# Optimization experiments

Measured on AMD Instinct MI355X. Metric: run time of the kernel, lower is better.

Reference implementation:

```python
import jax, jax.numpy as jnp
import numpy as np

B, D, H, A, T = 2048, 512, 512, 18, 16
W_SCALE = 1e-3


def setup_inputs() -> dict:
    key = jax.random.key(0)
    ks = jax.random.split(key, 7)
    xs = jax.random.normal(ks[0], (B, D), dtype=jnp.float32)
    task_id = jax.random.randint(ks[1], (B,), 0, T)
    action = jax.random.randint(ks[2], (B,), 0, A)
    W1 = jax.random.normal(ks[3], (T, D, H), dtype=jnp.float32) * W_SCALE
    b1 = jnp.zeros((T, H), dtype=jnp.float32)
    W2 = jax.random.normal(ks[4], (T, H, A), dtype=jnp.float32) * W_SCALE
    b2 = jnp.zeros((T, A), dtype=jnp.float32)
    return {"xs": xs, "W1": W1, "b1": b1, "W2": W2, "b2": b2,
            "task_id": task_id, "action": action}


def reference(xs, W1, b1, W2, b2, task_id, action):
    # MultiLinear fc1: gather per-sample weight by task_id, batched matmul
    h = jnp.einsum('bd,bdh->bh', xs, W1[task_id]) + b1[task_id]   # [B, H]
    h = jax.nn.relu(h)
    # MultiLinear fc2 -> logits
    logits = jnp.einsum('bh,bha->ba', h, W2[task_id]) + b2[task_id]  # [B, A]
    # Categorical log_prob / entropy
    logp = jax.nn.log_softmax(logits, axis=-1)                       # [B, A]
    log_pi_a = jnp.take_along_axis(logp, action[:, None], axis=-1)   # [B, 1]
    ent = -jnp.sum(jnp.exp(logp) * logp, axis=-1, keepdims=True)     # [B, 1]
    return action, log_pi_a, ent
```

## Files before the change

kernel.cpp:

```cpp
#include <hip/hip_runtime.h>
#include <math.h>

#define B_ 2048
#define D_ 512
#define H_ 512
#define A_ 18
#define T_ 16
#define MTF 16
#define MAXTILESF 144
#define NSLOT 24

typedef __attribute__((ext_vector_type(8))) short short8;
typedef __attribute__((ext_vector_type(4))) float f32x4;

#define W2T_OFF  (3 << 20)
#define W1T_OFF  (4 << 20)
#define WS_NEED  (12 << 20)

__device__ __forceinline__ unsigned short f2bf(float f) {
    union { float f; unsigned int u; } v; v.f = f;
    unsigned int u = v.u;
    return (unsigned short)((u + 0x7fffu + ((u >> 16) & 1u)) >> 16);
}

__global__ __launch_bounds__(256) void nk_prep(const float* __restrict__ W1,
                                               const float* __restrict__ W2,
                                               const int* __restrict__ task_id,
                                               unsigned short* __restrict__ w1t,
                                               unsigned short* __restrict__ w2t,
                                               int* __restrict__ wsi) {
    int bid = blockIdx.x;
    int tid = threadIdx.x;
    if (bid < 1024) {
        __shared__ float tile[64][65];
        int hx = bid & 7, dy = (bid >> 3) & 7, t = bid >> 6;
        int cx = tid & 63, ry = tid >> 6;
        const float* src = W1 + ((size_t)t * D_ + dy * 64) * H_ + hx * 64;
#pragma unroll
        for (int i = 0; i < 16; ++i) {
            int row = i * 4 + ry;
            tile[row][cx] = src[(size_t)row * H_ + cx];
        }
        __syncthreads();
        unsigned short* dst = w1t + ((size_t)t * H_ + hx * 64) * D_ + dy * 64;
        int c4 = tid & 15, hr0 = tid >> 4;
#pragma unroll
        for (int i = 0; i < 4; ++i) {
            int hr = hr0 + i * 16;
            unsigned short uu[4] = { f2bf(tile[c4 * 4 + 0][hr]), f2bf(tile[c4 * 4 + 1][hr]),
                                     f2bf(tile[c4 * 4 + 2][hr]), f2bf(tile[c4 * 4 + 3][hr]) };
            *(uint2*)(dst + (size_t)hr * D_ + c4 * 4) = *(const uint2*)uu;
        }
    } else if (bid < 1040) {
        int t = bid - 1024;
        const float* src = W2 + (size_t)t * H_ * A_;
        unsigned short* dst = w2t + (size_t)t * 32 * H_;
#pragma unroll
        for (int i = 0; i < 2; ++i) {
            int h = tid * 2 + i;
            float v[A_];
#pragma unroll
            for (int a = 0; a < A_; ++a) v[a] = src[(size_t)h * A_ + a];
#pragma unroll
            for (int a = 0; a < A_; ++a) dst[(size_t)a * H_ + h] = f2bf(v[a]);
#pragma unroll
            for (int a = A_; a < 32; ++a) dst[(size_t)a * H_ + h] = 0;
        }
    } else {
        __shared__ int cnt[T_], cur[T_], soff[T_];
        if (tid < T_) { cnt[tid] = 0; cur[tid] = 0; }
        __syncthreads();
        for (int b = tid; b < B_; b += 256) atomicAdd(&cnt[task_id[b]], 1);
        __syncthreads();
        if (tid == 0) {
            int off = 0;
            for (int t = 0; t < T_; ++t) {
                soff[t] = off; wsi[17 + t] = off;
                off += cnt[t];
            }
            wsi[17 + T_] = off;
        }
        __syncthreads();
        for (int b = tid; b < B_; b += 256) {
            int t = task_id[b];
            int pos = atomicAdd(&cur[t], 1);
            wsi[256 + soff[t] + pos] = b;
        }
    }
}

__global__ __launch_bounds__(512) void nk_fused(
        const float* __restrict__ xs,
        const unsigned short* __restrict__ w1t,
        const unsigned short* __restrict__ w2t,
        const float* __restrict__ b1, const float* __restrict__ b2,
        const int* __restrict__ action, float* __restrict__ out,
        const int* __restrict__ wsi) {
    __shared__ unsigned short x_lds[16][520];
    __shared__ unsigned short h_lds[16][520];
    __shared__ float lg_lds[16][34];
    __shared__ int sidx[16];

    int c = blockIdx.x;
    int tid = threadIdx.x, lane = tid & 63, w = tid >> 6;
    int r15 = lane & 15, kg = lane >> 4;

    int o0 = wsi[17 + c],     n0 = wsi[18 + c] - o0;
    int o1 = wsi[17 + c + 8], n1 = wsi[18 + c + 8] - o1;
    int nt0 = (n0 + 15) >> 4, nt1 = (n1 + 15) >> 4;
    int ntot = nt0 + nt1;

    for (int u = blockIdx.y; u < ntot; u += NSLOT) {
        int t, kt, off0, rT;
        if (u < nt0) { t = c; kt = u; off0 = o0; rT = n0; }
        else { t = c + 8; kt = u - nt0; off0 = o1; rT = n1; }
        int rowbase = off0 + kt * 16;
        int rows = rT - kt * 16; if (rows > 16) rows = 16;

        if (tid < 16) sidx[tid] = wsi[256 + rowbase + (tid < rows ? tid : rows - 1)];
        __syncthreads();

        {
            int row = tid >> 5, col = (tid & 31) * 16;
            const float* src = xs + (size_t)sidx[row] * D_ + col;
            float4 v0 = *(const float4*)(src);
            float4 v1 = *(const float4*)(src + 4);
            float4 v2 = *(const float4*)(src + 8);
            float4 v3 = *(const float4*)(src + 12);
            unsigned short uu[16] = {
                f2bf(v0.x), f2bf(v0.y), f2bf(v0.z), f2bf(v0.w),
                f2bf(v1.x), f2bf(v1.y), f2bf(v1.z), f2bf(v1.w),
                f2bf(v2.x), f2bf(v2.y), f2bf(v2.z), f2bf(v2.w),
                f2bf(v3.x), f2bf(v3.y), f2bf(v3.z), f2bf(v3.w) };
            *(uint4*)&x_lds[row][col]     = *(const uint4*)&uu[0];
            *(uint4*)&x_lds[row][col + 8] = *(const uint4*)&uu[8];
        }
        __syncthreads();

        const unsigned short* bbase = w1t + (size_t)t * H_ * D_ + kg * 8;
        const unsigned short* bp0 = bbase + (size_t)(w * 64 + r15) * D_;
        const unsigned short* bp1 = bp0 + (size_t)16 * D_;
        const unsigned short* bp2 = bp0 + (size_t)32 * D_;
        const unsigned short* bp3 = bp0 + (size_t)48 * D_;

        f32x4 acc0 = {0.f,0.f,0.f,0.f}, acc1 = {0.f,0.f,0.f,0.f};
        f32x4 acc2 = {0.f,0.f,0.f,0.f}, acc3 = {0.f,0.f,0.f,0.f};
#pragma unroll
        for (int ks = 0; ks < 16; ++ks) {
            short8 af = *(const short8*)&x_lds[r15][ks * 32 + kg * 8];
            short8 b0 = *(const short8*)(bp0 + ks * 32);
            short8 b1f = *(const short8*)(bp1 + ks * 32);
            short8 b2f = *(const short8*)(bp2 + ks * 32);
            short8 b3f = *(const short8*)(bp3 + ks * 32);
            acc0 = __builtin_amdgcn_mfma_f32_16x16x32_bf16(af, b0, acc0, 0, 0, 0);
            acc1 = __builtin_amdgcn_mfma_f32_16x16x32_bf16(af, b1f, acc1, 0, 0, 0);
            acc2 = __builtin_amdgcn_mfma_f32_16x16x32_bf16(af, b2f, acc2, 0, 0, 0);
            acc3 = __builtin_amdgcn_mfma_f32_16x16x32_bf16(af, b3f, acc3, 0, 0, 0);
        }

        int colb = w * 64 + r15;
        float bv0 = b1[t * H_ + colb];
        float bv1 = b1[t * H_ + colb + 16];
        float bv2 = b1[t * H_ + colb + 32];
        float bv3 = b1[t * H_ + colb + 48];
#pragma unroll
        for (int j = 0; j < 4; ++j) {
            int row = kg * 4 + j;
            float v;
            v = acc0[j] + bv0; h_lds[row][colb]      = f2bf(v > 0.f ? v : 0.f);
            v = acc1[j] + bv1; h_lds[row][colb + 16] = f2bf(v > 0.f ? v : 0.f);
            v = acc2[j] + bv2; h_lds[row][colb + 32] = f2bf(v > 0.f ? v : 0.f);
            v = acc3[j] + bv3; h_lds[row][colb + 48] = f2bf(v > 0.f ? v : 0.f);
        }
        __syncthreads();

        if (w < 2) {
            const unsigned short* wa = w2t + (size_t)t * 32 * H_
                                       + (size_t)(w * 16 + r15) * H_ + kg * 8;
            f32x4 c0 = {0.f,0.f,0.f,0.f};
#pragma unroll
            for (int ks = 0; ks < 16; ++ks) {
                short8 hf = *(const short8*)&h_lds[r15][ks * 32 + kg * 8];
                short8 w0 = *(const short8*)(wa + ks * 32);
                c0 = __builtin_amdgcn_mfma_f32_16x16x32_bf16(hf, w0, c0, 0, 0, 0);
            }
            int a = w * 16 + r15;
            float bb = (a < A_) ? b2[t * A_ + a] : 0.f;
#pragma unroll
            for (int j = 0; j < 4; ++j) {
                lg_lds[kg * 4 + j][a] = c0[j] + bb;
            }
        }
        __syncthreads();

        if (tid < rows) {
            int b = sidx[tid];
            float logits[A_];
            float m = -1e30f;
#pragma unroll
            for (int a = 0; a < A_; ++a) {
                logits[a] = lg_lds[tid][a];
                m = fmaxf(m, logits[a]);
            }
            float S = 0.f, sle = 0.f;
#pragma unroll
            for (int a = 0; a < A_; ++a) {
                float e = expf(logits[a] - m);
                S += e;
                sle += logits[a] * e;
            }
            float logZ = m + logf(S);
            int as = action[b];
            out[b] = (float)as;
            out[B_ + b] = logits[as] - logZ;
            out[2 * B_ + b] = logZ - sle / S;
        }
        __syncthreads();
    }
}


__global__ void nk_init(int* wsi) { int i = threadIdx.x; if (i < 50) wsi[i] = 0; }

__global__ void nk_count(const int* task_id, int* wsi) {
    int b = blockIdx.x * blockDim.x + threadIdx.x;
    if (b < B_) atomicAdd(&wsi[1 + task_id[b]], 1);
}

__global__ void nk_plan(int* wsi) {
    int off = 0, tot = 0;
    for (int t = 0; t < T_; ++t) {
        wsi[17 + t] = off;
        int cnt = wsi[1 + t];
        int nt = (cnt + MTF - 1) / MTF;
        for (int k = 0; k < nt; ++k) wsi[50 + tot++] = (t << 16) | k;
        off += cnt;
    }
    wsi[17 + T_] = off;
    wsi[0] = tot;
}

__global__ void nk_scatter(const int* task_id, int* wsi) {
    int b = blockIdx.x * blockDim.x + threadIdx.x;
    if (b < B_) {
        int t = task_id[b];
        int pos = atomicAdd(&wsi[34 + t], 1);
        wsi[256 + wsi[17 + t] + pos] = b;
    }
}

__global__ __launch_bounds__(512) void nk_main(
        const float* __restrict__ xs, const float* __restrict__ W1,
        const float* __restrict__ b1, const float* __restrict__ W2,
        const float* __restrict__ b2, const int* __restrict__ task_id,
        const int* __restrict__ action, float* __restrict__ out,
        const int* __restrict__ wsi) {
    __shared__ float tile[MTF][D_];
    __shared__ int sidx[MTF];
    int bid = blockIdx.x;
    if (bid >= wsi[0]) return;
    int code = wsi[50 + bid];
    int t = code >> 16, kt = code & 0xffff;
    int off0 = wsi[17 + t], off1 = wsi[17 + t + 1];
    int base = off0 + kt * MTF;
    int rows = off1 - base; if (rows > MTF) rows = MTF;
    int tid = threadIdx.x;
    if (tid < MTF) sidx[tid] = (tid < rows) ? wsi[256 + base + tid] : -1;
    __syncthreads();
    for (int i = 0; i < MTF; ++i) {
        int b = sidx[i];
        tile[i][tid] = (b >= 0) ? xs[(size_t)b * D_ + tid] : 0.f;
    }
    __syncthreads();
    const float* w1p = W1 + (size_t)t * D_ * H_ + tid;
    float acc[MTF];
#pragma unroll
    for (int i = 0; i < MTF; ++i) acc[i] = 0.f;
    for (int d = 0; d < D_; d += 4) {
        float w0 = w1p[(size_t)(d + 0) * H_];
        float w1v = w1p[(size_t)(d + 1) * H_];
        float w2v = w1p[(size_t)(d + 2) * H_];
        float w3v = w1p[(size_t)(d + 3) * H_];
#pragma unroll
        for (int i = 0; i < MTF; ++i) {
            float4 x = *(const float4*)&tile[i][d];
            float a0 = fmaf(x.x, w0, acc[i]);
            a0 = fmaf(x.y, w1v, a0);
            a0 = fmaf(x.z, w2v, a0);
            acc[i] = fmaf(x.w, w3v, a0);
        }
    }
    __syncthreads();
    float b1v = b1[t * H_ + tid];
#pragma unroll
    for (int i = 0; i < MTF; ++i) {
        float h = acc[i] + b1v;
        tile[i][tid] = h > 0.f ? h : 0.f;
    }
    __syncthreads();
    int g = tid >> 5, l = tid & 31;
    float lg[A_];
#pragma unroll
    for (int a = 0; a < A_; ++a) lg[a] = 0.f;
    const float* w2base = W2 + (size_t)t * H_ * A_;
    for (int hh = l; hh < H_; hh += 32) {
        float hv = tile[g][hh];
        const float* wrow = w2base + (size_t)hh * A_;
#pragma unroll
        for (int a = 0; a < A_; ++a) lg[a] = fmaf(hv, wrow[a], lg[a]);
    }
#pragma unroll
    for (int a = 0; a < A_; ++a) {
        lg[a] += __shfl_down(lg[a], 16, 32);
        lg[a] += __shfl_down(lg[a], 8, 32);
        lg[a] += __shfl_down(lg[a], 4, 32);
        lg[a] += __shfl_down(lg[a], 2, 32);
        lg[a] += __shfl_down(lg[a], 1, 32);
    }
    if (l == 0 && g < rows) {
        int b = sidx[g];
        float logits[A_];
        float m = -1e30f;
#pragma unroll
        for (int a = 0; a < A_; ++a) {
            logits[a] = lg[a] + b2[t * A_ + a];
            m = fmaxf(m, logits[a]);
        }
        float S = 0.f, sle = 0.f;
#pragma unroll
        for (int a = 0; a < A_; ++a) {
            float e = expf(logits[a] - m);
            S += e;
            sle += logits[a] * e;
        }
        float logZ = m + logf(S);
        int as = action[b];
        out[b] = (float)as;
        out[B_ + b] = logits[as] - logZ;
        out[2 * B_ + b] = logZ - sle / S;
    }
}

extern "C" void kernel_launch(void* const* d_in, const int* in_sizes, int n_in,
                              void* d_out, int out_size, void* d_ws, size_t ws_size,
                              hipStream_t stream) {
    const float* xs = (const float*)d_in[0];
    const float* W1 = (const float*)d_in[1];
    const float* b1 = (const float*)d_in[2];
    const float* W2 = (const float*)d_in[3];
    const float* b2 = (const float*)d_in[4];
    const int* task_id = (const int*)d_in[5];
    const int* action = (const int*)d_in[6];
    float* out = (float*)d_out;

    if (ws_size >= WS_NEED) {
        unsigned char* wsb = (unsigned char*)d_ws;
        int* wsi = (int*)d_ws;
        unsigned short* w2t = (unsigned short*)(wsb + W2T_OFF);
        unsigned short* w1t = (unsigned short*)(wsb + W1T_OFF);

        nk_prep<<<1041, 256, 0, stream>>>(W1, W2, task_id, w1t, w2t, wsi);
        nk_fused<<<dim3(8, NSLOT), 512, 0, stream>>>(xs, w1t, w2t, b1, b2,
                                                     action, out, wsi);
    } else {
        int* wsi = (int*)d_ws;
        nk_init<<<1, 64, 0, stream>>>(wsi);
        nk_count<<<(B_ + 255) / 256, 256, 0, stream>>>(task_id, wsi);
        nk_plan<<<1, 1, 0, stream>>>(wsi);
        nk_scatter<<<(B_ + 255) / 256, 256, 0, stream>>>(task_id, wsi);
        nk_main<<<MAXTILESF, 512, 0, stream>>>(xs, W1, b1, W2, b2, task_id, action, out, wsi);
    }
}
```

Measured before the change: 31.40 us.

## Split hidden dim across blocks with partial fc2 sums and separate softmax kernel

The fused per-16-row kernel is replaced by a GEMM kernel in which each block owns one task and a 32-column slice of the hidden dimension. It loops over that task's rows in 64-row tiles and writes partial fc2 logits to a workspace buffer. A new final kernel sums the 16 partials per row, adds b2, and computes log-softmax, log-prob and entropy. Each W1 slice is now loaded once per block instead of once per 16-row tile. The cost is an extra kernel launch, a partial-sum buffer round-trip through global memory, redundant conversion of x in every block, and a larger workspace requirement.

```diff
diff --git a/kernel.cpp b/kernel.cpp
--- a/kernel.cpp
+++ b/kernel.cpp
@@ -8,14 +8,14 @@
 #define T_ 16
 #define MTF 16
 #define MAXTILESF 144
-#define NSLOT 24
 
 typedef __attribute__((ext_vector_type(8))) short short8;
 typedef __attribute__((ext_vector_type(4))) float f32x4;
 
-#define W2T_OFF  (3 << 20)
-#define W1T_OFF  (4 << 20)
-#define WS_NEED  (12 << 20)
+#define PART_OFF 16384
+#define W2T_OFF  (5 << 20)
+#define W1T_OFF  (6 << 20)
+#define WS_NEED  (14 << 20)
 
 __device__ __forceinline__ unsigned short f2bf(float f) {
     union { float f; unsigned int u; } v; v.f = f;
@@ -89,134 +89,146 @@
     }
 }
 
-__global__ __launch_bounds__(512) void nk_fused(
+__global__ __launch_bounds__(256, 2) void nk_gemm(
         const float* __restrict__ xs,
         const unsigned short* __restrict__ w1t,
         const unsigned short* __restrict__ w2t,
-        const float* __restrict__ b1, const float* __restrict__ b2,
-        const int* __restrict__ action, float* __restrict__ out,
+        const float* __restrict__ b1,
+        float* __restrict__ part,
         const int* __restrict__ wsi) {
-    __shared__ unsigned short x_lds[16][520];
-    __shared__ unsigned short h_lds[16][520];
-    __shared__ float lg_lds[16][34];
-    __shared__ int sidx[16];
+    __shared__ unsigned short x_lds[64][520];
+    __shared__ unsigned short h_lds[64][36];
+    __shared__ int sidx[64];
 
     int c = blockIdx.x;
+    int slot = blockIdx.y;
+    int t = c + (slot >> 4) * 8;
+    int cq = slot & 15;
+    int c0 = cq * 32;
+
+    int o = wsi[17 + t];
+    int n = wsi[18 + t] - o;
+
     int tid = threadIdx.x, lane = tid & 63, w = tid >> 6;
     int r15 = lane & 15, kg = lane >> 4;
 
-    int o0 = wsi[17 + c],     n0 = wsi[18 + c] - o0;
-    int o1 = wsi[17 + c + 8], n1 = wsi[18 + c + 8] - o1;
-    int nt0 = (n0 + 15) >> 4, nt1 = (n1 + 15) >> 4;
-    int ntot = nt0 + nt1;
-
-    for (int u = blockIdx.y; u < ntot; u += NSLOT) {
-        int t, kt, off0, rT;
-        if (u < nt0) { t = c; kt = u; off0 = o0; rT = n0; }
-        else { t = c + 8; kt = u - nt0; off0 = o1; rT = n1; }
-        int rowbase = off0 + kt * 16;
-        int rows = rT - kt * 16; if (rows > 16) rows = 16;
-
-        if (tid < 16) sidx[tid] = wsi[256 + rowbase + (tid < rows ? tid : rows - 1)];
+    const unsigned short* bp0 = w1t + (size_t)t * H_ * D_ + (size_t)(c0 + r15) * D_ + kg * 8;
+    const unsigned short* bp1 = bp0 + (size_t)16 * D_;
+    const unsigned short* wa0 = w2t + (size_t)t * 32 * H_ + (size_t)r15 * H_ + c0 + kg * 8;
+    const unsigned short* wa1 = wa0 + (size_t)16 * H_;
+    float bv0 = b1[t * H_ + c0 + r15];
+    float bv1 = b1[t * H_ + c0 + 16 + r15];
+
+    for (int mb = 0; mb * 64 < n; ++mb) {
+        int rowbase = o + mb * 64;
+        int rows = n - mb * 64; if (rows > 64) rows = 64;
+
+        if (tid < 64) sidx[tid] = wsi[256 + rowbase + (tid < rows ? tid : rows - 1)];
         __syncthreads();
 
         {
-            int row = tid >> 5, col = (tid & 31) * 16;
-            const float* src = xs + (size_t)sidx[row] * D_ + col;
-            float4 v0 = *(const float4*)(src);
-            float4 v1 = *(const float4*)(src + 4);
-            float4 v2 = *(const float4*)(src + 8);
-            float4 v3 = *(const float4*)(src + 12);
-            unsigned short uu[16] = {
-                f2bf(v0.x), f2bf(v0.y), f2bf(v0.z), f2bf(v0.w),
-                f2bf(v1.x), f2bf(v1.y), f2bf(v1.z), f2bf(v1.w),
-                f2bf(v2.x), f2bf(v2.y), f2bf(v2.z), f2bf(v2.w),
-                f2bf(v3.x), f2bf(v3.y), f2bf(v3.z), f2bf(v3.w) };
-            *(uint4*)&x_lds[row][col]     = *(const uint4*)&uu[0];
-            *(uint4*)&x_lds[row][col + 8] = *(const uint4*)&uu[8];
-        }
-        __syncthreads();
-
-        const unsigned short* bbase = w1t + (size_t)t * H_ * D_ + kg * 8;
-        const unsigned short* bp0 = bbase + (size_t)(w * 64 + r15) * D_;
-        const unsigned short* bp1 = bp0 + (size_t)16 * D_;
-        const unsigned short* bp2 = bp0 + (size_t)32 * D_;
-        const unsigned short* bp3 = bp0 + (size_t)48 * D_;
+            int row = tid >> 2, cb = (tid & 3) * 128;
+            const float* src = xs + (size_t)sidx[row] * D_ + cb;
+#pragma unroll
+            for (int j = 0; j < 8; ++j) {
+                float4 v0 = *(const float4*)(src + j * 16);
+                float4 v1 = *(const float4*)(src + j * 16 + 4);
+                float4 v2 = *(const float4*)(src + j * 16 + 8);
+                float4 v3 = *(const float4*)(src + j * 16 + 12);
+                unsigned short uu[16] = {
+                    f2bf(v0.x), f2bf(v0.y), f2bf(v0.z), f2bf(v0.w),
+                    f2bf(v1.x), f2bf(v1.y), f2bf(v1.z), f2bf(v1.w),
+                    f2bf(v2.x), f2bf(v2.y), f2bf(v2.z), f2bf(v2.w),
+                    f2bf(v3.x), f2bf(v3.y), f2bf(v3.z), f2bf(v3.w) };
+                *(uint4*)&x_lds[row][cb + j * 16]     = *(const uint4*)&uu[0];
+                *(uint4*)&x_lds[row][cb + j * 16 + 8] = *(const uint4*)&uu[8];
+            }
+        }
+        __syncthreads();
 
         f32x4 acc0 = {0.f,0.f,0.f,0.f}, acc1 = {0.f,0.f,0.f,0.f};
-        f32x4 acc2 = {0.f,0.f,0.f,0.f}, acc3 = {0.f,0.f,0.f,0.f};
 #pragma unroll
         for (int ks = 0; ks < 16; ++ks) {
-            short8 af = *(const short8*)&x_lds[r15][ks * 32 + kg * 8];
+            short8 af = *(const short8*)&x_lds[w * 16 + r15][ks * 32 + kg * 8];
             short8 b0 = *(const short8*)(bp0 + ks * 32);
             short8 b1f = *(const short8*)(bp1 + ks * 32);
-            short8 b2f = *(const short8*)(bp2 + ks * 32);
-            short8 b3f = *(const short8*)(bp3 + ks * 32);
             acc0 = __builtin_amdgcn_mfma_f32_16x16x32_bf16(af, b0, acc0, 0, 0, 0);
             acc1 = __builtin_amdgcn_mfma_f32_16x16x32_bf16(af, b1f, acc1, 0, 0, 0);
-            acc2 = __builtin_amdgcn_mfma_f32_16x16x32_bf16(af, b2f, acc2, 0, 0, 0);
-            acc3 = __builtin_amdgcn_mfma_f32_16x16x32_bf16(af, b3f, acc3, 0, 0, 0);
-        }
-
-        int colb = w * 64 + r15;
-        float bv0 = b1[t * H_ + colb];
-        float bv1 = b1[t * H_ + colb + 16];
-        float bv2 = b1[t * H_ + colb + 32];
-        float bv3 = b1[t * H_ + colb + 48];
+        }
+
 #pragma unroll
         for (int j = 0; j < 4; ++j) {
-            int row = kg * 4 + j;
+            int row = w * 16 + kg * 4 + j;
             float v;
-            v = acc0[j] + bv0; h_lds[row][colb]      = f2bf(v > 0.f ? v : 0.f);
-            v = acc1[j] + bv1; h_lds[row][colb + 16] = f2bf(v > 0.f ? v : 0.f);
-            v = acc2[j] + bv2; h_lds[row][colb + 32] = f2bf(v > 0.f ? v : 0.f);
-            v = acc3[j] + bv3; h_lds[row][colb + 48] = f2bf(v > 0.f ? v : 0.f);
-        }
-        __syncthreads();
-
-        if (w < 2) {
-            const unsigned short* wa = w2t + (size_t)t * 32 * H_
-                                       + (size_t)(w * 16 + r15) * H_ + kg * 8;
-            f32x4 c0 = {0.f,0.f,0.f,0.f};
-#pragma unroll
-            for (int ks = 0; ks < 16; ++ks) {
-                short8 hf = *(const short8*)&h_lds[r15][ks * 32 + kg * 8];
-                short8 w0 = *(const short8*)(wa + ks * 32);
-                c0 = __builtin_amdgcn_mfma_f32_16x16x32_bf16(hf, w0, c0, 0, 0, 0);
+            v = acc0[j] + bv0; h_lds[row][r15]      = f2bf(v > 0.f ? v : 0.f);
+            v = acc1[j] + bv1; h_lds[row][16 + r15] = f2bf(v > 0.f ? v : 0.f);
+        }
+        __syncthreads();
+
+        {
+            short8 hf = *(const short8*)&h_lds[w * 16 + r15][kg * 8];
+            short8 w2f0 = *(const short8*)wa0;
+            short8 w2f1 = *(const short8*)wa1;
+            f32x4 p0 = {0.f,0.f,0.f,0.f}, p1 = {0.f,0.f,0.f,0.f};
+            p0 = __builtin_amdgcn_mfma_f32_16x16x32_bf16(hf, w2f0, p0, 0, 0, 0);
+            p1 = __builtin_amdgcn_mfma_f32_16x16x32_bf16(hf, w2f1, p1, 0, 0, 0);
+#pragma unroll
+            for (int j = 0; j < 4; ++j) {
+                int lrow = w * 16 + kg * 4 + j;
+                if (lrow < rows) {
+                    float* pp = part + ((size_t)(rowbase + lrow) * 16 + cq) * 32;
+                    pp[r15] = p0[j];
+                    pp[16 + r15] = p1[j];
+                }
             }
-            int a = w * 16 + r15;
-            float bb = (a < A_) ? b2[t * A_ + a] : 0.f;
-#pragma unroll
-            for (int j = 0; j < 4; ++j) {
-                lg_lds[kg * 4 + j][a] = c0[j] + bb;
-            }
-        }
-        __syncthreads();
-
-        if (tid < rows) {
-            int b = sidx[tid];
-            float logits[A_];
-            float m = -1e30f;
-#pragma unroll
-            for (int a = 0; a < A_; ++a) {
-                logits[a] = lg_lds[tid][a];
-                m = fmaxf(m, logits[a]);
-            }
-            float S = 0.f, sle = 0.f;
-#pragma unroll
-            for (int a = 0; a < A_; ++a) {
-                float e = expf(logits[a] - m);
-                S += e;
-                sle += logits[a] * e;
-            }
-            float logZ = m + logf(S);
-            int as = action[b];
-            out[b] = (float)as;
-            out[B_ + b] = logits[as] - logZ;
-            out[2 * B_ + b] = logZ - sle / S;
-        }
-        __syncthreads();
-    }
+        }
+        __syncthreads();
+    }
+}
+
+__global__ __launch_bounds__(256) void nk_final(const float* __restrict__ part,
+                                                const float* __restrict__ b2,
+                                                const int* __restrict__ action,
+                                                float* __restrict__ out,
+                                                const int* __restrict__ wsi) {
+    int r = blockIdx.x * 256 + threadIdx.x;
+    if (r >= B_) return;
+    int t = 0;
+#pragma unroll
+    for (int i = 1; i < T_; ++i) t += (r >= wsi[17 + i]) ? 1 : 0;
+    int b = wsi[256 + r];
+
+    float logits[A_];
+#pragma unroll
+    for (int a = 0; a < A_; ++a) logits[a] = b2[t * A_ + a];
+    const float* pr = part + (size_t)r * 16 * 32;
+#pragma unroll
+    for (int cq = 0; cq < 16; ++cq) {
+        const float* pc = pr + cq * 32;
+#pragma unroll
+        for (int a4 = 0; a4 < 5; ++a4) {
+            float4 v = *(const float4*)(pc + a4 * 4);
+            if (a4 * 4 + 0 < A_) logits[a4 * 4 + 0] += v.x;
+            if (a4 * 4 + 1 < A_) logits[a4 * 4 + 1] += v.y;
+            if (a4 * 4 + 2 < A_) logits[a4 * 4 + 2] += v.z;
+            if (a4 * 4 + 3 < A_) logits[a4 * 4 + 3] += v.w;
+        }
+    }
+    float m = -1e30f;
+#pragma unroll
+    for (int a = 0; a < A_; ++a) m = fmaxf(m, logits[a]);
+    float S = 0.f, sle = 0.f;
+#pragma unroll
+    for (int a = 0; a < A_; ++a) {
+        float e = expf(logits[a] - m);
+        S += e;
+        sle += logits[a] * e;
+    }
+    float logZ = m + logf(S);
+    int as = action[b];
+    out[b] = (float)as;
+    out[B_ + b] = logits[as] - logZ;
+    out[2 * B_ + b] = logZ - sle / S;
 }
 
 
@@ -356,12 +368,13 @@
     if (ws_size >= WS_NEED) {
         unsigned char* wsb = (unsigned char*)d_ws;
         int* wsi = (int*)d_ws;
+        float* part = (float*)(wsb + PART_OFF);
         unsigned short* w2t = (unsigned short*)(wsb + W2T_OFF);
         unsigned short* w1t = (unsigned short*)(wsb + W1T_OFF);
 
         nk_prep<<<1041, 256, 0, stream>>>(W1, W2, task_id, w1t, w2t, wsi);
-        nk_fused<<<dim3(8, NSLOT), 512, 0, stream>>>(xs, w1t, w2t, b1, b2,
-                                                     action, out, wsi);
+        nk_gemm<<<dim3(8, 32), 256, 0, stream>>>(xs, w1t, w2t, b1, part, wsi);
+        nk_final<<<(B_ + 255) / 256, 256, 0, stream>>>(part, b2, action, out, wsi);
     } else {
         int* wsi = (int*)d_ws;
         nk_init<<<1, 64, 0, stream>>>(wsi);
```

After: 48.84 us. 1.56x slower.

## Prefetch fc1 MFMA operands and split fc2 K-dimension across four waves

Applied to the files above, without the earlier changes.

The fc1 MFMA loop now software-pipelines its operand loads, fetching the next k-step's x fragment and W1 fragments before issuing the current MFMAs, so global-load latency can hide behind matrix work. The fc2 logits stage moves from two waves each covering the full K=512 to four waves that each handle a quarter of K for both 16-column output tiles. Partial sums go to a per-wave LDS buffer and are reduced, with the bias added, in the softmax thread. This trades more LDS traffic, higher register pressure from the prefetch buffers, and a serial 4-way reduction for a shorter fc2 critical path.

```diff
diff --git a/kernel.cpp b/kernel.cpp
--- a/kernel.cpp
+++ b/kernel.cpp
@@ -98,7 +98,7 @@
         const int* __restrict__ wsi) {
     __shared__ unsigned short x_lds[16][520];
     __shared__ unsigned short h_lds[16][520];
-    __shared__ float lg_lds[16][34];
+    __shared__ float lg_lds[4][16][36];
     __shared__ int sidx[16];
 
     int c = blockIdx.x;
@@ -145,17 +145,29 @@
 
         f32x4 acc0 = {0.f,0.f,0.f,0.f}, acc1 = {0.f,0.f,0.f,0.f};
         f32x4 acc2 = {0.f,0.f,0.f,0.f}, acc3 = {0.f,0.f,0.f,0.f};
+
+        short8 a_cur = *(const short8*)&x_lds[r15][kg * 8];
+        short8 b0c = *(const short8*)(bp0);
+        short8 b1c = *(const short8*)(bp1);
+        short8 b2c = *(const short8*)(bp2);
+        short8 b3c = *(const short8*)(bp3);
 #pragma unroll
         for (int ks = 0; ks < 16; ++ks) {
-            short8 af = *(const short8*)&x_lds[r15][ks * 32 + kg * 8];
-            short8 b0 = *(const short8*)(bp0 + ks * 32);
-            short8 b1f = *(const short8*)(bp1 + ks * 32);
-            short8 b2f = *(const short8*)(bp2 + ks * 32);
-            short8 b3f = *(const short8*)(bp3 + ks * 32);
-            acc0 = __builtin_amdgcn_mfma_f32_16x16x32_bf16(af, b0, acc0, 0, 0, 0);
-            acc1 = __builtin_amdgcn_mfma_f32_16x16x32_bf16(af, b1f, acc1, 0, 0, 0);
-            acc2 = __builtin_amdgcn_mfma_f32_16x16x32_bf16(af, b2f, acc2, 0, 0, 0);
-            acc3 = __builtin_amdgcn_mfma_f32_16x16x32_bf16(af, b3f, acc3, 0, 0, 0);
+            short8 a_nxt, b0n, b1n, b2n, b3n;
+            if (ks < 15) {
+                a_nxt = *(const short8*)&x_lds[r15][(ks + 1) * 32 + kg * 8];
+                b0n = *(const short8*)(bp0 + (ks + 1) * 32);
+                b1n = *(const short8*)(bp1 + (ks + 1) * 32);
+                b2n = *(const short8*)(bp2 + (ks + 1) * 32);
+                b3n = *(const short8*)(bp3 + (ks + 1) * 32);
+            }
+            acc0 = __builtin_amdgcn_mfma_f32_16x16x32_bf16(a_cur, b0c, acc0, 0, 0, 0);
+            acc1 = __builtin_amdgcn_mfma_f32_16x16x32_bf16(a_cur, b1c, acc1, 0, 0, 0);
+            acc2 = __builtin_amdgcn_mfma_f32_16x16x32_bf16(a_cur, b2c, acc2, 0, 0, 0);
+            acc3 = __builtin_amdgcn_mfma_f32_16x16x32_bf16(a_cur, b3c, acc3, 0, 0, 0);
+            if (ks < 15) {
+                a_cur = a_nxt; b0c = b0n; b1c = b1n; b2c = b2n; b3c = b3n;
+            }
         }
 
         int colb = w * 64 + r15;
@@ -174,21 +186,25 @@
         }
         __syncthreads();
 
-        if (w < 2) {
-            const unsigned short* wa = w2t + (size_t)t * 32 * H_
-                                       + (size_t)(w * 16 + r15) * H_ + kg * 8;
-            f32x4 c0 = {0.f,0.f,0.f,0.f};
-#pragma unroll
-            for (int ks = 0; ks < 16; ++ks) {
+        if (w < 4) {
+            const unsigned short* wa0 = w2t + (size_t)t * 32 * H_
+                                        + (size_t)r15 * H_ + kg * 8;
+            const unsigned short* wa1 = wa0 + (size_t)16 * H_;
+            f32x4 c0 = {0.f,0.f,0.f,0.f}, c1 = {0.f,0.f,0.f,0.f};
+#pragma unroll
+            for (int j = 0; j < 4; ++j) {
+                int ks = w * 4 + j;
                 short8 hf = *(const short8*)&h_lds[r15][ks * 32 + kg * 8];
-                short8 w0 = *(const short8*)(wa + ks * 32);
+                short8 w0 = *(const short8*)(wa0 + ks * 32);
+                short8 w1f = *(const short8*)(wa1 + ks * 32);
                 c0 = __builtin_amdgcn_mfma_f32_16x16x32_bf16(hf, w0, c0, 0, 0, 0);
-            }
-            int a = w * 16 + r15;
-            float bb = (a < A_) ? b2[t * A_ + a] : 0.f;
+                c1 = __builtin_amdgcn_mfma_f32_16x16x32_bf16(hf, w1f, c1, 0, 0, 0);
+            }
 #pragma unroll
             for (int j = 0; j < 4; ++j) {
-                lg_lds[kg * 4 + j][a] = c0[j] + bb;
+                int row = kg * 4 + j;
+                lg_lds[w][row][r15] = c0[j];
+                lg_lds[w][row][16 + r15] = c1[j];
             }
         }
         __syncthreads();
@@ -199,8 +215,10 @@
             float m = -1e30f;
 #pragma unroll
             for (int a = 0; a < A_; ++a) {
-                logits[a] = lg_lds[tid][a];
-                m = fmaxf(m, logits[a]);
+                float v = lg_lds[0][tid][a] + lg_lds[1][tid][a]
+                        + lg_lds[2][tid][a] + lg_lds[3][tid][a] + b2[t * A_ + a];
+                logits[a] = v;
+                m = fmaxf(m, v);
             }
             float S = 0.f, sle = 0.f;
 #pragma unroll
```

Result: slower. 32.04 us (+2.1%).
